# Kernel tuning notes

Hardware: AMD Instinct MI355X
Metric: run time of the kernel (lower is better)

Reference implementation:

```python
import jax, jax.numpy as jnp
import numpy as np

TABLE = 16777216  # maxGridFeatId[-1]
FEAT = 4          # eachGridFeatDim
IN_DIR = 16       # in_dim_dir
H_COLOR = 8       # hidden_dim_color


def setup_inputs() -> dict:
    key = jax.random.key(0)
    k1, k2, k3, k4, k5 = jax.random.split(key, 5)
    B, N = 32768, 128
    x = jax.random.randint(k1, (B, N, 2), 0, TABLE, dtype=jnp.int64) if jax.config.jax_enable_x64 else jax.random.randint(k1, (B, N, 2), 0, TABLE, dtype=jnp.int32)
    d = jax.random.normal(k2, (B, IN_DIR), dtype=jnp.float32)
    gridWeight = jax.random.uniform(k3, (TABLE, FEAT), dtype=jnp.float32)  # torch.rand init
    in_color = IN_DIR + 2 * (FEAT - 1)  # 16 + 6 = 22
    # nn.Linear(in,out,bias=False); stored here already transposed for h @ W
    W0 = jax.random.uniform(k4, (in_color, H_COLOR), dtype=jnp.float32, minval=-1.0, maxval=1.0) / jnp.sqrt(in_color)
    W1 = jax.random.uniform(k5, (H_COLOR, 3), dtype=jnp.float32, minval=-1.0, maxval=1.0) / jnp.sqrt(H_COLOR)
    return {"x": x, "d": d, "gridWeight": gridWeight, "W0": W0, "W1": W1}


def reference(x, d, gridWeight, W0, W1):
    B, N, _ = x.shape
    # gather grid features: [B*N*2, FEAT] -> [B, 2N, FEAT]
    feat = jnp.take(gridWeight, x.reshape(-1), axis=0).reshape(B, 2 * N, FEAT)
    sigma12 = feat[..., 0].reshape(B, N, 2)
    sigma = jax.nn.sigmoid(sigma12[..., 0] * sigma12[..., 1])       # [B, N]
    geo_feat = feat[..., 1:].reshape(B, N, 2 * (FEAT - 1))          # [B, N, 6]
    d_tiled = jnp.broadcast_to(d[:, None, :], (B, N, d.shape[-1]))  # [B, N, 16]
    h = jnp.concatenate([d_tiled, geo_feat], axis=-1)               # [B, N, 22]
    h = jax.nn.relu(h @ W0)                                         # [B, N, 8]
    color = jax.nn.sigmoid(h @ W1)                                  # [B, N, 3]
    # transmittance before each sample: cumprod of (1 - sigma) shifted by one
    T = jnp.cumprod(jnp.concatenate([jnp.ones((B, 1), sigma.dtype),
                                     1.0 - sigma[:, :-1]], axis=1), axis=1)
    w = T * sigma                                                   # [B, N]
    rgb = jnp.einsum('bn,bnc->bc', w, color)                        # [B, 3]
    return sigma, rgb
```

## Files before the change

kernel.cpp:

```cpp
#include <hip/hip_runtime.h>


__global__ __launch_bounds__(128) void surf_kernel(
    const int*   __restrict__ x,
    const float* __restrict__ dvec,
    const float* __restrict__ grid,
    const float* __restrict__ W0,
    const float* __restrict__ W1,
    float*       __restrict__ sigma_out,
    float*       __restrict__ rgb_out,
    int N)
{
    const int b    = blockIdx.x;
    const int n    = threadIdx.x;
    const int lane = n & 63;
    const int wv   = n >> 6;

    __shared__ float W0s[22 * 8];
    __shared__ float W1s[8 * 3];
    __shared__ float dsh[16];
    __shared__ float dW0[8];
    __shared__ float scanb[128];
    __shared__ float wtot[2];
    __shared__ float rsum[2][3];

    if (n < 88) { W0s[n] = W0[n]; W0s[n + 88] = W0[n + 88]; }
    if (n < 24) W1s[n] = W1[n];
    if (n < 16) dsh[n] = dvec[(size_t)b * 16 + n];
    __syncthreads();

    if (n < 8) {
        float acc = 0.f;
        #pragma unroll
        for (int i = 0; i < 16; ++i) acc += dsh[i] * W0s[i * 8 + n];
        dW0[n] = acc;
    }

    const int2 idx = ((const int2*)x)[(size_t)b * N + n];
    const float4 fa = ((const float4*)grid)[idx.x];
    const float4 fb = ((const float4*)grid)[idx.y];

    const float s = 1.f / (1.f + __expf(-(fa.x * fb.x)));
    const float geo[6] = { fa.y, fa.z, fa.w, fb.y, fb.z, fb.w };

    __syncthreads();

    float h8[8];
    #pragma unroll
    for (int j = 0; j < 8; ++j) {
        float acc = dW0[j];
        #pragma unroll
        for (int i = 0; i < 6; ++i) acc += geo[i] * W0s[(16 + i) * 8 + j];
        h8[j] = fmaxf(acc, 0.f);
    }
    float col[3];
    #pragma unroll
    for (int c = 0; c < 3; ++c) {
        float acc = 0.f;
        #pragma unroll
        for (int k = 0; k < 8; ++k) acc += h8[k] * W1s[k * 3 + c];
        col[c] = 1.f / (1.f + __expf(-acc));
    }

    float p = 1.f - s;
    #pragma unroll
    for (int off = 1; off < 64; off <<= 1) {
        float o = __shfl_up(p, off, 64);
        if (lane >= off) p *= o;
    }
    if (lane == 63) wtot[wv] = p;
    __syncthreads();
    if (wv == 1) p *= wtot[0];
    scanb[n] = p;
    __syncthreads();

    const float T = (n == 0) ? 1.f : scanb[n - 1];
    const float w = T * s;

    sigma_out[(size_t)b * N + n] = s;

    float r0 = w * col[0], r1 = w * col[1], r2 = w * col[2];
    #pragma unroll
    for (int off = 32; off > 0; off >>= 1) {
        r0 += __shfl_down(r0, off, 64);
        r1 += __shfl_down(r1, off, 64);
        r2 += __shfl_down(r2, off, 64);
    }
    if (lane == 0) { rsum[wv][0] = r0; rsum[wv][1] = r1; rsum[wv][2] = r2; }
    __syncthreads();
    if (n == 0) {
        rgb_out[b * 3 + 0] = rsum[0][0] + rsum[1][0];
        rgb_out[b * 3 + 1] = rsum[0][1] + rsum[1][1];
        rgb_out[b * 3 + 2] = rsum[0][2] + rsum[1][2];
    }
}

extern "C" void kernel_launch(void* const* d_in, const int* in_sizes, int n_in,
                              void* d_out, int out_size, void* d_ws, size_t ws_size,
                              hipStream_t stream) {
    const int*   x    = (const int*)d_in[0];
    const float* dvec = (const float*)d_in[1];
    const float* grid = (const float*)d_in[2];
    const float* W0   = (const float*)d_in[3];
    const float* W1   = (const float*)d_in[4];

    const int B = in_sizes[1] / 16;
    const int N = in_sizes[0] / (2 * B);

    float* sigma_out = (float*)d_out;
    float* rgb_out   = sigma_out + (size_t)B * N;

    surf_kernel<<<B, N, 0, stream>>>(x, dvec, grid, W0, W1, sigma_out, rgb_out, N);
}
```

Before: 166.5 us.

## Map one wavefront per ray with two samples per lane, removing shared memory and barriers

Each ray is now handled by a single 64-lane wavefront, with each lane processing two samples, and four rays are packed into a 256-thread block. This removes the shared-memory staging and block-level barriers, and the scan and reduction become purely intra-wavefront. Index loads are 16-byte nontemporal and sigma stores are 8-byte nontemporal. Weights are read directly from global memory through uniform loads. N is now hardcoded to 128, so other sample counts are no longer supported.

```diff
diff --git a/kernel.cpp b/kernel.cpp
--- a/kernel.cpp
+++ b/kernel.cpp
@@ -1,7 +1,12 @@
 #include <hip/hip_runtime.h>
 
 
-__global__ __launch_bounds__(128) void surf_kernel(
+typedef int   iv4 __attribute__((ext_vector_type(4)));
+typedef float fv2 __attribute__((ext_vector_type(2)));
+
+constexpr int ROWS_PER_BLOCK = 4;
+
+__global__ __launch_bounds__(256) void surf_kernel(
     const int*   __restrict__ x,
     const float* __restrict__ dvec,
     const float* __restrict__ grid,
@@ -9,89 +14,87 @@
     const float* __restrict__ W1,
     float*       __restrict__ sigma_out,
     float*       __restrict__ rgb_out,
-    int N)
+    int B)
 {
-    const int b    = blockIdx.x;
-    const int n    = threadIdx.x;
-    const int lane = n & 63;
-    const int wv   = n >> 6;
+    const int lane = threadIdx.x & 63;
+    const int wv   = threadIdx.x >> 6;
+    const int row  = __builtin_amdgcn_readfirstlane(blockIdx.x * ROWS_PER_BLOCK + wv);
+    if (row >= B) return;
 
-    __shared__ float W0s[22 * 8];
-    __shared__ float W1s[8 * 3];
-    __shared__ float dsh[16];
-    __shared__ float dW0[8];
-    __shared__ float scanb[128];
-    __shared__ float wtot[2];
-    __shared__ float rsum[2][3];
+    const iv4 idx = __builtin_nontemporal_load(
+        (const iv4*)x + (size_t)row * 64 + lane);
+    const float4 fa0 = ((const float4*)grid)[idx.x];
+    const float4 fb0 = ((const float4*)grid)[idx.y];
+    const float4 fa1 = ((const float4*)grid)[idx.z];
+    const float4 fb1 = ((const float4*)grid)[idx.w];
 
-    if (n < 88) { W0s[n] = W0[n]; W0s[n + 88] = W0[n + 88]; }
-    if (n < 24) W1s[n] = W1[n];
-    if (n < 16) dsh[n] = dvec[(size_t)b * 16 + n];
-    __syncthreads();
-
-    if (n < 8) {
-        float acc = 0.f;
+    const float* dp = dvec + (size_t)row * 16;
+    float dW0[8];
+    #pragma unroll
+    for (int j = 0; j < 8; ++j) dW0[j] = 0.f;
+    #pragma unroll
+    for (int i = 0; i < 16; ++i) {
+        const float di = dp[i];
         #pragma unroll
-        for (int i = 0; i < 16; ++i) acc += dsh[i] * W0s[i * 8 + n];
-        dW0[n] = acc;
+        for (int j = 0; j < 8; ++j)
+            dW0[j] = fmaf(di, W0[i * 8 + j], dW0[j]);
     }
 
-    const int2 idx = ((const int2*)x)[(size_t)b * N + n];
-    const float4 fa = ((const float4*)grid)[idx.x];
-    const float4 fb = ((const float4*)grid)[idx.y];
-
-    const float s = 1.f / (1.f + __expf(-(fa.x * fb.x)));
-    const float geo[6] = { fa.y, fa.z, fa.w, fb.y, fb.z, fb.w };
-
-    __syncthreads();
-
-    float h8[8];
+    float s[2], col[2][3];
     #pragma unroll
-    for (int j = 0; j < 8; ++j) {
-        float acc = dW0[j];
+    for (int q = 0; q < 2; ++q) {
+        const float4 fa = q ? fa1 : fa0;
+        const float4 fb = q ? fb1 : fb0;
+        s[q] = 1.f / (1.f + __expf(-(fa.x * fb.x)));
+        const float geo[6] = { fa.y, fa.z, fa.w, fb.y, fb.z, fb.w };
+        float h[8];
         #pragma unroll
-        for (int i = 0; i < 6; ++i) acc += geo[i] * W0s[(16 + i) * 8 + j];
-        h8[j] = fmaxf(acc, 0.f);
-    }
-    float col[3];
-    #pragma unroll
-    for (int c = 0; c < 3; ++c) {
-        float acc = 0.f;
+        for (int j = 0; j < 8; ++j) {
+            float acc = dW0[j];
+            #pragma unroll
+            for (int i = 0; i < 6; ++i)
+                acc = fmaf(geo[i], W0[(16 + i) * 8 + j], acc);
+            h[j] = fmaxf(acc, 0.f);
+        }
         #pragma unroll
-        for (int k = 0; k < 8; ++k) acc += h8[k] * W1s[k * 3 + c];
-        col[c] = 1.f / (1.f + __expf(-acc));
+        for (int c = 0; c < 3; ++c) {
+            float acc = 0.f;
+            #pragma unroll
+            for (int k = 0; k < 8; ++k)
+                acc = fmaf(h[k], W1[k * 3 + c], acc);
+            col[q][c] = 1.f / (1.f + __expf(-acc));
+        }
     }
 
-    float p = 1.f - s;
+    const float q0 = 1.f - s[0];
+    float p = q0 * (1.f - s[1]);
     #pragma unroll
     for (int off = 1; off < 64; off <<= 1) {
-        float o = __shfl_up(p, off, 64);
+        const float o = __shfl_up(p, off, 64);
         if (lane >= off) p *= o;
     }
-    if (lane == 63) wtot[wv] = p;
-    __syncthreads();
-    if (wv == 1) p *= wtot[0];
-    scanb[n] = p;
-    __syncthreads();
+    float T0 = __shfl_up(p, 1, 64);
+    if (lane == 0) T0 = 1.f;
+    const float T1 = T0 * q0;
+    const float w0 = T0 * s[0];
+    const float w1 = T1 * s[1];
 
-    const float T = (n == 0) ? 1.f : scanb[n - 1];
-    const float w = T * s;
+    const fv2 sv = { s[0], s[1] };
+    __builtin_nontemporal_store(sv, (fv2*)sigma_out + (size_t)row * 64 + lane);
 
-    sigma_out[(size_t)b * N + n] = s;
-
-    float r0 = w * col[0], r1 = w * col[1], r2 = w * col[2];
+    float r0 = fmaf(w0, col[0][0], w1 * col[1][0]);
+    float r1 = fmaf(w0, col[0][1], w1 * col[1][1]);
+    float r2 = fmaf(w0, col[0][2], w1 * col[1][2]);
     #pragma unroll
     for (int off = 32; off > 0; off >>= 1) {
         r0 += __shfl_down(r0, off, 64);
         r1 += __shfl_down(r1, off, 64);
         r2 += __shfl_down(r2, off, 64);
     }
-    if (lane == 0) { rsum[wv][0] = r0; rsum[wv][1] = r1; rsum[wv][2] = r2; }
-    __syncthreads();
-    if (n == 0) {
-        rgb_out[b * 3 + 0] = rsum[0][0] + rsum[1][0];
-        rgb_out[b * 3 + 1] = rsum[0][1] + rsum[1][1];
-        rgb_out[b * 3 + 2] = rsum[0][2] + rsum[1][2];
+    if (lane == 0) {
+        rgb_out[row * 3 + 0] = r0;
+        rgb_out[row * 3 + 1] = r1;
+        rgb_out[row * 3 + 2] = r2;
     }
 }
 
@@ -105,10 +108,11 @@
     const float* W1   = (const float*)d_in[4];
 
     const int B = in_sizes[1] / 16;
-    const int N = in_sizes[0] / (2 * B);
 
     float* sigma_out = (float*)d_out;
-    float* rgb_out   = sigma_out + (size_t)B * N;
+    float* rgb_out   = sigma_out + (size_t)B * 128;
 
-    surf_kernel<<<B, N, 0, stream>>>(x, dvec, grid, W0, W1, sigma_out, rgb_out, N);
+    const int grid_blocks = (B + ROWS_PER_BLOCK - 1) / ROWS_PER_BLOCK;
+    surf_kernel<<<grid_blocks, ROWS_PER_BLOCK * 64, 0, stream>>>(
+        x, dvec, grid, W0, W1, sigma_out, rgb_out, B);
 }
```

Result: no change. 167.7 us (+0.7%).
